# Kernel tuning notes

Hardware: AMD Instinct MI355X
Metric: run time of the kernel (lower is better)

Reference implementation:

```python
import jax, jax.numpy as jnp
from jax import lax
import numpy as np

RADIUS = 0.1
NSAMPLE = 32
STRIDE = 3
ED_NSAMPLE = 10


def _sqdist(a, b):
    # a: [B,M,3], b: [B,N,3] -> [B,M,N] squared euclidean distance
    return (jnp.sum(a * a, -1)[:, :, None] + jnp.sum(b * b, -1)[:, None, :]
            - 2.0 * jnp.einsum('bmc,bnc->bmn', a, b))


def setup_inputs() -> dict:
    key = jax.random.key(0)
    ks = jax.random.split(key, 16)
    B, N = 8, 4096
    s = 0.05
    inp = {
        'data': jax.random.normal(ks[0], (B, N, 3), dtype=jnp.float32),
        'numpoints': N,
        # stem MLP 3 -> 64
        'W_stem': jax.random.normal(ks[1], (3, 64), dtype=jnp.float32) * s,
        'b_stem': jnp.zeros((64,), jnp.float32),
        # SA shared MLP (3 dp + 64 fj) -> 128
        'W_sa': jax.random.normal(ks[2], (67, 128), dtype=jnp.float32) * s,
        'b_sa': jnp.zeros((128,), jnp.float32),
        # FP MLP (128 interp + 64 skip) -> 64
        'W_fp': jax.random.normal(ks[3], (192, 64), dtype=jnp.float32) * s,
        'b_fp': jnp.zeros((64,), jnp.float32),
        # eigen-feature MLP 3 -> 4 -> 4
        'W_e1': jax.random.normal(ks[4], (3, 4), dtype=jnp.float32) * s,
        'b_e1': jnp.zeros((4,), jnp.float32),
        'W_e2': jax.random.normal(ks[5], (4, 4), dtype=jnp.float32) * s,
        'b_e2': jnp.zeros((4,), jnp.float32),
        # conv_final 1x1: 68 -> 64, + BN affine
        'W_fin': jax.random.normal(ks[6], (68, 64), dtype=jnp.float32) * s,
        'b_fin': jnp.zeros((64,), jnp.float32),
        'gamma': jnp.ones((64,), jnp.float32),
        'beta': jnp.zeros((64,), jnp.float32),
    }
    return inp


def reference(data, numpoints, W_stem, b_stem, W_sa, b_sa, W_fp, b_fp,
              W_e1, b_e1, W_e2, b_e2, W_fin, b_fin, gamma, beta):
    B, N, _ = data.shape
    b_ix = jnp.arange(B)[:, None, None]

    # ---------- encoder: stem MLP ----------
    f0 = jax.nn.relu(data @ W_stem + b_stem)  # [B,N,64]

    # set abstraction: stride-subsample centers, ball query, dp_fj, MLP, max
    sub_idx = jnp.arange(0, N, STRIDE)
    new_xyz = data[:, sub_idx]                 # [B,M,3]
    d2 = _sqdist(new_xyz, data)                # [B,M,N]
    col = jnp.arange(N, dtype=jnp.int32)
    valid = d2 < RADIUS * RADIUS
    keys = jnp.where(valid, col, N + col)      # first-valid ball query ordering
    negk, _ = lax.top_k(-keys, NSAMPLE)
    idx = -negk                                # [B,M,ns]
    first = idx[..., :1]                       # self point always valid
    idx = jnp.where(idx >= N, first, idx)
    g_xyz = data[b_ix, idx]                    # [B,M,ns,3]
    dp = (g_xyz - new_xyz[:, :, None, :]) / RADIUS  # normalize_dp
    g_f = f0[b_ix, idx]                        # [B,M,ns,64]
    feat = jnp.concatenate([dp, g_f], -1)      # [B,M,ns,67]
    h = jax.nn.relu(feat @ W_sa + b_sa)        # [B,M,ns,128]
    f_sub = jnp.max(h, axis=2)                 # [B,M,128]

    # ---------- decoder: 3-NN inverse-distance feature propagation ----------
    d2f = _sqdist(data, new_xyz)               # [B,N,M]
    negd, nn = lax.top_k(-d2f, 3)
    w = 1.0 / (-negd + 1e-8)
    w = w / jnp.sum(w, -1, keepdims=True)      # [B,N,3]
    nbr_f = f_sub[b_ix, nn]                    # [B,N,3,128]
    interp = jnp.einsum('bnk,bnkc->bnc', w, nbr_f)
    f = jax.nn.relu(jnp.concatenate([interp, f0], -1) @ W_fp + b_fp)  # [B,N,64]

    # ---------- KNN covariance eigen-features ----------
    d2e = _sqdist(data, data)                  # [B,N,N]
    _, gidx = lax.top_k(-d2e, ED_NSAMPLE)      # [B,N,k]
    nbr = data[b_ix, gidx]                     # [B,N,k,3]
    cen = nbr - jnp.mean(nbr, axis=2, keepdims=True)
    cov = jnp.einsum('bnkc,bnkd->bncd', cen, cen) / ED_NSAMPLE  # [B,N,3,3]
    eig = jnp.linalg.eigvalsh(cov)             # [B,N,3] ascending
    ef = jax.nn.relu(eig @ W_e1 + b_e1) @ W_e2 + b_e2  # [B,N,4]

    # ---------- fused 1x1 conv + BN (training-mode stats) + relu ----------
    z_in = jnp.concatenate([f, ef], -1)        # [B,N,68]
    zc = z_in @ W_fin + b_fin                  # [B,N,64]
    mu = jnp.mean(zc, axis=(0, 1))
    var = jnp.var(zc, axis=(0, 1))
    z = jax.nn.relu((zc - mu) * lax.rsqrt(var + 1e-5) * gamma + beta)
    z = jnp.transpose(z, (0, 2, 1))            # [B,64,N]
    return (data, z)
```

## Files before the change

### kernel.cpp

```cpp
#include <hip/hip_runtime.h>
#include <stdint.h>

#define BB 8
#define NN 4096
#define MM 1366
#define NS 32
#define RAD2 0.01f
#define NGRP 64
#define KW 8

__device__ __forceinline__ float rl(float v, int l) {
    return __int_as_float(__builtin_amdgcn_readlane(__float_as_int(v), l));
}
__device__ __forceinline__ uint32_t um(uint32_t a, uint32_t b) { return a < b ? a : b; }
__device__ __forceinline__ uint32_t ux(uint32_t a, uint32_t b) { return a > b ? a : b; }
__device__ __forceinline__ uint32_t um3(uint32_t a, uint32_t b, uint32_t c) { return um(um(a, b), c); }

__device__ __forceinline__ void mrg2(uint32_t* kk, uint32_t s0, uint32_t s1) {
    uint32_t n0 = um(kk[0], s0);
    uint32_t n1 = um3(kk[1], ux(kk[0], s0), s1);
    uint32_t n2 = um3(kk[2], ux(kk[1], s0), ux(kk[0], s1));
    uint32_t n3 = um3(kk[3], ux(kk[2], s0), ux(kk[1], s1));
    uint32_t n4 = um3(kk[4], ux(kk[3], s0), ux(kk[2], s1));
    uint32_t n5 = um3(kk[5], ux(kk[4], s0), ux(kk[3], s1));
    uint32_t n6 = um3(kk[6], ux(kk[5], s0), ux(kk[4], s1));
    uint32_t n7 = um3(kk[7], ux(kk[6], s0), ux(kk[5], s1));
    uint32_t n8 = um3(kk[8], ux(kk[7], s0), ux(kk[6], s1));
    uint32_t n9 = um3(kk[9], ux(kk[8], s0), ux(kk[7], s1));
    kk[0]=n0; kk[1]=n1; kk[2]=n2; kk[3]=n3; kk[4]=n4;
    kk[5]=n5; kk[6]=n6; kk[7]=n7; kk[8]=n8; kk[9]=n9;
}

__device__ __forceinline__ void mrg4(uint32_t* kk, uint32_t s0, uint32_t s1,
                                     uint32_t s2, uint32_t s3) {
    uint32_t n0 = um(kk[0], s0);
    uint32_t n1 = um3(kk[1], ux(kk[0], s0), s1);
    uint32_t n2 = um(um3(kk[2], ux(kk[1], s0), ux(kk[0], s1)), s2);
    uint32_t n3 = um3(um3(kk[3], ux(kk[2], s0), ux(kk[1], s1)), ux(kk[0], s2), s3);
    uint32_t n4 = um3(um3(kk[4], ux(kk[3], s0), ux(kk[2], s1)), ux(kk[1], s2), ux(kk[0], s3));
    uint32_t n5 = um3(um3(kk[5], ux(kk[4], s0), ux(kk[3], s1)), ux(kk[2], s2), ux(kk[1], s3));
    uint32_t n6 = um3(um3(kk[6], ux(kk[5], s0), ux(kk[4], s1)), ux(kk[3], s2), ux(kk[2], s3));
    uint32_t n7 = um3(um3(kk[7], ux(kk[6], s0), ux(kk[5], s1)), ux(kk[4], s2), ux(kk[3], s3));
    uint32_t n8 = um3(um3(kk[8], ux(kk[7], s0), ux(kk[6], s1)), ux(kk[5], s2), ux(kk[4], s3));
    uint32_t n9 = um3(um3(kk[9], ux(kk[8], s0), ux(kk[7], s1)), ux(kk[6], s2), ux(kk[5], s3));
    kk[0]=n0; kk[1]=n1; kk[2]=n2; kk[3]=n3; kk[4]=n4;
    kk[5]=n5; kk[6]=n6; kk[7]=n7; kk[8]=n8; kk[9]=n9;
}

__device__ __forceinline__ void srt4(uint32_t& a, uint32_t& b, uint32_t& c, uint32_t& d) {
    uint32_t t0 = um(a, b), t1 = ux(a, b), t2 = um(c, d), t3 = ux(c, d);
    uint32_t s0 = um(t0, t2), m0 = ux(t0, t2), m1 = um(t1, t3), s3 = ux(t1, t3);
    a = s0; b = um(m0, m1); c = ux(m0, m1); d = s3;
}

__device__ __forceinline__ uint32_t spr3(uint32_t v) {
    v = (v | (v << 4)) & 0xC3u;
    v = (v | (v << 2)) & 0x249u;
    return v;
}

__global__ __launch_bounds__(256) void k_stem(const float* __restrict__ data,
                                              const float* __restrict__ Ws,
                                              const float* __restrict__ bs,
                                              float* __restrict__ f0,
                                              float* __restrict__ out,
                                              float4* __restrict__ cand4) {
    int blk = blockIdx.x;
    if (blk >= (BB * NN * 64) / 256) {
        int t = (blk - (BB * NN * 64) / 256) * 256 + threadIdx.x;
        float x = data[t * 3], y = data[t * 3 + 1], z = data[t * 3 + 2];
        out[t * 3] = x; out[t * 3 + 1] = y; out[t * 3 + 2] = z;
        cand4[t] = make_float4(x, y, z, x * x + y * y + z * z);
        return;
    }
    int t = blk * 256 + threadIdx.x;
    int c = t & 63;
    int r = t >> 6;
    const float* d = data + r * 3;
    float acc = bs[c];
    acc = fmaf(d[0], Ws[c], acc);
    acc = fmaf(d[1], Ws[64 + c], acc);
    acc = fmaf(d[2], Ws[128 + c], acc);
    f0[t] = fmaxf(acc, 0.f);
}

__global__ __launch_bounds__(256) void k_sort(const float4* __restrict__ cand4,
                                              float4* __restrict__ cand4s,
                                              uint32_t* __restrict__ perm,
                                              float4* __restrict__ gbox) {
    __shared__ uint32_t cnt[4096];
    __shared__ uint32_t part[256];
    int b = blockIdx.x, t = threadIdx.x;
    const float4* cb = cand4 + b * NN;
    for (int i = t; i < 4096; i += 256) cnt[i] = 0;
    __syncthreads();
    uint32_t cid[16];
    #pragma unroll
    for (int u = 0; u < 16; ++u) {
        float4 c = cb[u * 256 + t];
        int ix = (int)floorf((c.x + 4.f) * 2.f);
        int iy = (int)floorf((c.y + 4.f) * 2.f);
        int iz = (int)floorf((c.z + 4.f) * 2.f);
        ix = ix < 0 ? 0 : (ix > 15 ? 15 : ix);
        iy = iy < 0 ? 0 : (iy > 15 ? 15 : iy);
        iz = iz < 0 ? 0 : (iz > 15 ? 15 : iz);
        uint32_t m = spr3((uint32_t)ix) | (spr3((uint32_t)iy) << 1) | (spr3((uint32_t)iz) << 2);
        cid[u] = m;
        atomicAdd(&cnt[m], 1u);
    }
    __syncthreads();
    uint32_t c16[16];
    uint32_t s = 0;
    #pragma unroll
    for (int u = 0; u < 16; ++u) { c16[u] = cnt[t * 16 + u]; s += c16[u]; }
    part[t] = s;
    __syncthreads();
    for (int off = 1; off < 256; off <<= 1) {
        uint32_t v = (t >= off) ? part[t - off] : 0u;
        __syncthreads();
        part[t] += v;
        __syncthreads();
    }
    uint32_t run = part[t] - s;
    #pragma unroll
    for (int u = 0; u < 16; ++u) { cnt[t * 16 + u] = run; run += c16[u]; }
    __syncthreads();
    #pragma unroll
    for (int u = 0; u < 16; ++u) {
        int p = u * 256 + t;
        uint32_t pos = atomicAdd(&cnt[cid[u]], 1u);
        cand4s[b * NN + pos] = cb[p];
        perm[b * NN + pos] = (uint32_t)p;
    }
    __syncthreads();
    if (t < NGRP) {
        float4 mn = make_float4(1e30f, 1e30f, 1e30f, 0.f);
        float4 mx = make_float4(-1e30f, -1e30f, -1e30f, 0.f);
        for (int j = 0; j < 64; ++j) {
            float4 c = cand4s[b * NN + t * 64 + j];
            mn.x = fminf(mn.x, c.x); mn.y = fminf(mn.y, c.y); mn.z = fminf(mn.z, c.z);
            mx.x = fmaxf(mx.x, c.x); mx.y = fmaxf(mx.y, c.y); mx.z = fmaxf(mx.z, c.z);
        }
        gbox[(b * NGRP + t) * 2]     = mn;
        gbox[(b * NGRP + t) * 2 + 1] = mx;
    }
}

__global__ __launch_bounds__(512) void k_knn(const float4* __restrict__ cand4s,
                                             const uint32_t* __restrict__ perm,
                                             const float4* __restrict__ gbox,
                                             uint32_t* __restrict__ mrg) {
    __shared__ float4 sBox[2 * NGRP];
    __shared__ uint32_t sKK[KW][64][10];
    int t = threadIdx.x, w = t >> 6, lane = t & 63;
    int gw = blockIdx.x;
    int b = gw >> 6;
    int g = gw & (NGRP - 1);
    for (int i = t; i < 2 * NGRP; i += 512) sBox[i] = gbox[b * 2 * NGRP + i];
    __syncthreads();
    const float4* cs = cand4s + b * NN;
    const uint32_t* ps = perm + b * NN;
    float4 me = cs[g * 64 + lane];
    uint32_t mo = ps[g * 64 + lane];
    float px = me.x, py = me.y, pz = me.z, pa = me.w;
    uint32_t kk[10];
    #pragma unroll
    for (int r = 0; r < 10; ++r) kk[r] = 0xFFFFFF00u + r;

    auto scan_packets = [&](int jg, int j0, int j1) {
        const float4* cp = cs + jg * 64;
        const uint4* pq = (const uint4*)(ps + jg * 64);
        for (int j = j0; j < j1; ++j) {
            float4 ca  = cp[j * 4];
            float4 cbv = cp[j * 4 + 1];
            float4 cc  = cp[j * 4 + 2];
            float4 cd  = cp[j * 4 + 3];
            uint4 pm = pq[j];
            float da  = fmaxf(fmaf(-2.f, fmaf(pz, ca.z,  fmaf(py, ca.y,  px * ca.x)),  pa + ca.w),  0.f);
            float db_ = fmaxf(fmaf(-2.f, fmaf(pz, cbv.z, fmaf(py, cbv.y, px * cbv.x)), pa + cbv.w), 0.f);
            float dc  = fmaxf(fmaf(-2.f, fmaf(pz, cc.z,  fmaf(py, cc.y,  px * cc.x)),  pa + cc.w),  0.f);
            float dd  = fmaxf(fmaf(-2.f, fmaf(pz, cd.z,  fmaf(py, cd.y,  px * cd.x)),  pa + cd.w),  0.f);
            uint32_t ka = (__float_as_uint(da)  & 0xFFFFF000u) | pm.x;
            uint32_t kb = (__float_as_uint(db_) & 0xFFFFF000u) | pm.y;
            uint32_t kc = (__float_as_uint(dc)  & 0xFFFFF000u) | pm.z;
            uint32_t kd = (__float_as_uint(dd)  & 0xFFFFF000u) | pm.w;
            uint32_t mn4 = um(um(ka, kb), um(kc, kd));
            if (__ballot(mn4 < kk[9])) {
                srt4(ka, kb, kc, kd);
                mrg4(kk, ka, kb, kc, kd);
            }
        }
    };
    auto bound = [&]() {
        uint32_t kb9 = kk[9] & 0xFFFFF000u;
        float u2 = (kb9 >= 0x7F000000u) ? 1e30f : __uint_as_float(kb9 + 0x1000u);
        #pragma unroll
        for (int off = 1; off < 64; off <<= 1) u2 = fmaxf(u2, __shfl_xor(u2, off));
        return u2;
    };

    scan_packets(g, w * 2, w * 2 + 2);
    float ub = bound();
    float4 amn = sBox[g * 2], amx = sBox[g * 2 + 1];
    float4 bmn = sBox[lane * 2], bmx = sBox[lane * 2 + 1];
    float bx = fmaxf(fmaxf(amn.x - bmx.x, bmn.x - amx.x), 0.f);
    float by = fmaxf(fmaxf(amn.y - bmx.y, bmn.y - amx.y), 0.f);
    float bz = fmaxf(fmaxf(amn.z - bmx.z, bmn.z - amx.z), 0.f);
    float bdj = fmaf(bx, bx, fmaf(by, by, bz * bz));
    if (lane == g) bdj = 1e30f;
    for (int rank = 0; rank < NGRP - 1; ++rank) {
        float mind = bdj;
        #pragma unroll
        for (int off = 1; off < 64; off <<= 1) mind = fminf(mind, __shfl_xor(mind, off));
        if (!(mind < ub * 1.0005f)) break;
        unsigned long long mm = __ballot(bdj == mind);
        int jl = (int)__builtin_ctzll(mm);
        if (lane == jl) bdj = 1e30f;
        if ((rank & (KW - 1)) == w) {
            scan_packets(jl, 0, 16);
            ub = bound();
        }
    }
    if (w > 0) {
        #pragma unroll
        for (int r = 0; r < 10; ++r) sKK[w][lane][r] = kk[r];
    }
    __syncthreads();
    if (w == 0) {
        for (int ww = 1; ww < KW; ++ww) {
            uint32_t s[10];
            #pragma unroll
            for (int r = 0; r < 10; ++r) s[r] = sKK[ww][lane][r];
            mrg4(kk, s[0], s[1], s[2], s[3]);
            mrg4(kk, s[4], s[5], s[6], s[7]);
            mrg2(kk, s[8], s[9]);
        }
        int gp = b * NN + (int)mo;
        #pragma unroll
        for (int r = 0; r < 10; ++r) mrg[r * (BB * NN) + gp] = kk[r];
    }
}

__device__ __forceinline__ void jrot(float& app, float& aqq, float& apq,
                                     float& arp, float& arq) {
    float ap = apq;
    if (fabsf(ap) > 1e-32f) {
        float th = (aqq - app) / (2.f * ap);
        float t = 1.f / (fabsf(th) + sqrtf(th * th + 1.f));
        t = th < 0.f ? -t : t;
        float c = 1.f / sqrtf(t * t + 1.f);
        float s = t * c;
        app = app - t * ap;
        aqq = aqq + t * ap;
        apq = 0.f;
        float rp = arp, rq = arq;
        arp = c * rp - s * rq;
        arq = s * rp + c * rq;
    }
}

__global__ __launch_bounds__(256) void k_knn_eig(const float4* __restrict__ cand4,
                                                 const uint32_t* __restrict__ mrg,
                                                 const float* __restrict__ We1,
                                                 const float* __restrict__ be1,
                                                 const float* __restrict__ We2,
                                                 const float* __restrict__ be2,
                                                 float* __restrict__ ef) {
    int t = blockIdx.x * 256 + threadIdx.x;
    int b = t >> 12;
    const float4* cb = cand4 + b * NN;
    uint32_t kk[10];
    #pragma unroll
    for (int r = 0; r < 10; ++r) kk[r] = mrg[r * (BB * NN) + t];
    float xs[10], ys[10], zs[10];
    float mx = 0.f, my = 0.f, mz = 0.f;
    #pragma unroll
    for (int r = 0; r < 10; ++r) {
        int n = (int)(kk[r] & 0xFFFu);
        float4 cr = cb[n];
        xs[r] = cr.x; ys[r] = cr.y; zs[r] = cr.z;
        mx += xs[r]; my += ys[r]; mz += zs[r];
    }
    mx *= 0.1f; my *= 0.1f; mz *= 0.1f;
    float a00 = 0, a01 = 0, a02 = 0, a11 = 0, a12 = 0, a22 = 0;
    #pragma unroll
    for (int r = 0; r < 10; ++r) {
        float x = xs[r] - mx, y = ys[r] - my, z = zs[r] - mz;
        a00 = fmaf(x, x, a00); a01 = fmaf(x, y, a01); a02 = fmaf(x, z, a02);
        a11 = fmaf(y, y, a11); a12 = fmaf(y, z, a12); a22 = fmaf(z, z, a22);
    }
    a00 *= 0.1f; a01 *= 0.1f; a02 *= 0.1f; a11 *= 0.1f; a12 *= 0.1f; a22 *= 0.1f;
    #pragma unroll
    for (int sweep = 0; sweep < 6; ++sweep) {
        jrot(a00, a11, a01, a02, a12);
        jrot(a00, a22, a02, a01, a12);
        jrot(a11, a22, a12, a01, a02);
    }
    float e0 = a00, e1 = a11, e2 = a22, tmp;
    if (e0 > e1) { tmp = e0; e0 = e1; e1 = tmp; }
    if (e1 > e2) { tmp = e1; e1 = e2; e2 = tmp; }
    if (e0 > e1) { tmp = e0; e0 = e1; e1 = tmp; }
    float tt[4];
    #pragma unroll
    for (int i = 0; i < 4; ++i) {
        float v = be1[i];
        v = fmaf(e0, We1[i], v);
        v = fmaf(e1, We1[4 + i], v);
        v = fmaf(e2, We1[8 + i], v);
        tt[i] = fmaxf(v, 0.f);
    }
    #pragma unroll
    for (int i = 0; i < 4; ++i) {
        float v = be2[i];
        v = fmaf(tt[0], We2[i], v);
        v = fmaf(tt[1], We2[4 + i], v);
        v = fmaf(tt[2], We2[8 + i], v);
        v = fmaf(tt[3], We2[12 + i], v);
        ef[t * 4 + i] = v;
    }
}

__global__ __launch_bounds__(256) void k_sa(const float4* __restrict__ cand4,
                                            const float* __restrict__ data,
                                            const float* __restrict__ f0,
                                            const uint32_t* __restrict__ mrg,
                                            const float* __restrict__ Wsa,
                                            const float* __restrict__ bsa,
                                            float* __restrict__ fsub) {
    __shared__ float2 sW[67 * 64];
    __shared__ int sIdx[4][NS];
    for (int i = threadIdx.x; i < 67 * 64; i += 256) {
        int k = i >> 6, c = i & 63;
        sW[i] = make_float2(Wsa[k * 128 + c], Wsa[k * 128 + 64 + c]);
    }
    __syncthreads();
    int wv = threadIdx.x >> 6, lane = threadIdx.x & 63;
    int gm = blockIdx.x * 4 + wv;
    if (gm >= BB * MM) return;
    int b = gm / MM, m = gm - b * MM;
    const float4* cb4 = cand4 + b * NN;
    const float* db = data + b * NN * 3;
    float4 cen = cb4[3 * m];
    float cx = cen.x, cy = cen.y, cz = cen.z, sa = cen.w;

    int cnt;
    bool fallback;
    {
        float d2l = 1e30f;
        int idxl = 0;
        if (lane < 10) {
            uint32_t key = mrg[lane * (BB * NN) + b * NN + 3 * m];
            idxl = (int)(key & 0xFFFu);
            float4 c = cb4[idxl];
            float dot = fmaf(cz, c.z, fmaf(cy, c.y, cx * c.x));
            d2l = (sa + c.w) - 2.f * dot;
        }
        bool valid = (lane < 10) && (d2l < RAD2);
        unsigned long long mask = __ballot(valid);
        if (valid) sIdx[wv][__popcll(mask & ((1ull << lane) - 1ull))] = idxl;
        cnt = __popcll(mask);
        fallback = rl(d2l, 9) < RAD2 * 1.0005f;
    }
    if (fallback) {
        cnt = 0;
        for (int base = 0; base < NN; base += 64) {
            int n = base + lane;
            float4 c = cb4[n];
            float dot = fmaf(cz, c.z, fmaf(cy, c.y, cx * c.x));
            float d2 = (sa + c.w) - 2.f * dot;
            bool valid = d2 < RAD2;
            unsigned long long mask = __ballot(valid);
            if (valid) {
                int pos = cnt + __popcll(mask & ((1ull << lane) - 1ull));
                if (pos < NS) sIdx[wv][pos] = n;
            }
            cnt += __popcll(mask);
            if (cnt >= NS) break;
        }
    }
    int scnt = cnt < NS ? cnt : NS;

    float cl = lane == 0 ? cx : (lane == 1 ? cy : cz);
    float hb0 = bsa[lane], hb1 = bsa[64 + lane];
    float m0 = 0.f, m1 = 0.f;

    for (int s0 = 0; s0 < scnt; s0 += 4) {
        float fr[4], fr2[4];
        #pragma unroll
        for (int u = 0; u < 4; ++u) {
            int s = s0 + u;
            if (s >= scnt) s = 0;
            int nj = sIdx[wv][s];
            int fb = (b * NN + nj) * 64;
            float v;
            if (lane >= 3) v = f0[fb + lane - 3];
            else           v = (db[nj * 3 + lane] - cl) * 10.0f;
            fr[u] = v;
            fr2[u] = (lane < 3) ? f0[fb + 61 + lane] : 0.f;
        }
        float h0[4], h1[4];
        #pragma unroll
        for (int u = 0; u < 4; ++u) { h0[u] = hb0; h1[u] = hb1; }
        for (int k = 0; k < 64; ++k) {
            float2 w = sW[k * 64 + lane];
            #pragma unroll
            for (int u = 0; u < 4; ++u) {
                float fv = rl(fr[u], k);
                h0[u] = fmaf(fv, w.x, h0[u]);
                h1[u] = fmaf(fv, w.y, h1[u]);
            }
        }
        #pragma unroll
        for (int k = 64; k < 67; ++k) {
            float2 w = sW[k * 64 + lane];
            #pragma unroll
            for (int u = 0; u < 4; ++u) {
                float fv = rl(fr2[u], k - 64);
                h0[u] = fmaf(fv, w.x, h0[u]);
                h1[u] = fmaf(fv, w.y, h1[u]);
            }
        }
        #pragma unroll
        for (int u = 0; u < 4; ++u) {
            m0 = fmaxf(m0, fmaxf(h0[u], 0.f));
            m1 = fmaxf(m1, fmaxf(h1[u], 0.f));
        }
    }
    fsub[gm * 128 + lane] = m0;
    fsub[gm * 128 + 64 + lane] = m1;
}

__global__ __launch_bounds__(512) void k_interp(const float4* __restrict__ cand4,
                                                const float* __restrict__ fsub,
                                                float* __restrict__ itp) {
    __shared__ float4 sC[MM];
    __shared__ float sMD[8][64][3];
    __shared__ int   sMI[8][64][3];
    __shared__ float sWts[64][3];
    __shared__ int   sNbr[64][3];
    int t = threadIdx.x, wv = t >> 6, lane = t & 63;
    int blk = blockIdx.x;
    int b = blk >> 6;
    int pbase = (blk & 63) * 64;
    const float4* cb4 = cand4 + b * NN;
    for (int m = t; m < MM; m += 512) sC[m] = cb4[3 * m];
    __syncthreads();
    int p = pbase + lane;
    float4 pm = cb4[p];
    float px = pm.x, py = pm.y, pz = pm.z, pa = pm.w;
    float d0 = 1e30f, d1 = 1e30f, d2v = 1e30f;
    int n0 = 0, n1 = 0, n2 = 0;
    int ms = wv * 171, me = ms + 171 < MM ? ms + 171 : MM;
    for (int m = ms; m < me; ++m) {
        float4 c = sC[m];
        float dd = (pa + c.w) - 2.f * (px * c.x + py * c.y + pz * c.z);
        if (dd < d2v) {
            if (dd < d1) {
                d2v = d1; n2 = n1;
                if (dd < d0) { d1 = d0; n1 = n0; d0 = dd; n0 = m; }
                else         { d1 = dd; n1 = m; }
            } else { d2v = dd; n2 = m; }
        }
    }
    sMD[wv][lane][0] = d0; sMD[wv][lane][1] = d1; sMD[wv][lane][2] = d2v;
    sMI[wv][lane][0] = n0; sMI[wv][lane][1] = n1; sMI[wv][lane][2] = n2;
    __syncthreads();
    if (wv == 0) {
        d0 = sMD[0][lane][0]; d1 = sMD[0][lane][1]; d2v = sMD[0][lane][2];
        n0 = sMI[0][lane][0]; n1 = sMI[0][lane][1]; n2 = sMI[0][lane][2];
        for (int w = 1; w < 8; ++w) {
            #pragma unroll
            for (int r = 0; r < 3; ++r) {
                float dd = sMD[w][lane][r];
                int mm = sMI[w][lane][r];
                if (dd < d2v) {
                    if (dd < d1) {
                        d2v = d1; n2 = n1;
                        if (dd < d0) { d1 = d0; n1 = n0; d0 = dd; n0 = mm; }
                        else         { d1 = dd; n1 = mm; }
                    } else { d2v = dd; n2 = mm; }
                }
            }
        }
        float w0 = 1.f / (d0 + 1e-8f), w1 = 1.f / (d1 + 1e-8f), w2 = 1.f / (d2v + 1e-8f);
        float ws = w0 + w1 + w2;
        sWts[lane][0] = w0 / ws; sWts[lane][1] = w1 / ws; sWts[lane][2] = w2 / ws;
        sNbr[lane][0] = n0; sNbr[lane][1] = n1; sNbr[lane][2] = n2;
    }
    __syncthreads();
    for (int i = wv * 8; i < wv * 8 + 8; ++i) {
        float a0 = sWts[i][0], a1 = sWts[i][1], a2 = sWts[i][2];
        const float* r0 = fsub + (b * MM + sNbr[i][0]) * 128;
        const float* r1 = fsub + (b * MM + sNbr[i][1]) * 128;
        const float* r2 = fsub + (b * MM + sNbr[i][2]) * 128;
        float v0 = fmaf(a2, r2[lane], fmaf(a1, r1[lane], a0 * r0[lane]));
        float v1 = fmaf(a2, r2[64 + lane], fmaf(a1, r1[64 + lane], a0 * r0[64 + lane]));
        int row = b * NN + pbase + i;
        itp[row * 128 + lane] = v0;
        itp[row * 128 + 64 + lane] = v1;
    }
}

__global__ __launch_bounds__(256) void k_fp(const float* __restrict__ itp,
                                            const float* __restrict__ f0,
                                            const float* __restrict__ W,
                                            const float* __restrict__ bias,
                                            float* __restrict__ outf) {
    __shared__ float sW[192 * 64];
    for (int i = threadIdx.x; i < 192 * 64; i += 256) sW[i] = W[i];
    __syncthreads();
    int lane = threadIdx.x & 63;
    int wv = threadIdx.x >> 6;
    float bb = bias[lane];
    int rowbase = blockIdx.x * 64 + wv * 16;
    for (int it = 0; it < 4; ++it) {
        int r = rowbase + it * 4;
        float fa[4], fbv[4], fc[4], acc[4];
        #pragma unroll
        for (int u = 0; u < 4; ++u) {
            fa[u]  = itp[(r + u) * 128 + lane];
            fbv[u] = itp[(r + u) * 128 + 64 + lane];
            fc[u]  = f0[(r + u) * 64 + lane];
            acc[u] = bb;
        }
        #pragma unroll
        for (int k = 0; k < 192; ++k) {
            float w = sW[k * 64 + lane];
            #pragma unroll
            for (int u = 0; u < 4; ++u) {
                float fv = k < 64 ? rl(fa[u], k)
                         : (k < 128 ? rl(fbv[u], k - 64) : rl(fc[u], k - 128));
                acc[u] = fmaf(fv, w, acc[u]);
            }
        }
        #pragma unroll
        for (int u = 0; u < 4; ++u)
            outf[(r + u) * 64 + lane] = fmaxf(acc[u], 0.f);
    }
}

__global__ __launch_bounds__(256) void k_fin(const float* __restrict__ fb,
                                             const float* __restrict__ efb,
                                             const float* __restrict__ W,
                                             const float* __restrict__ bias,
                                             float* __restrict__ zc) {
    __shared__ float sW[68 * 64];
    for (int i = threadIdx.x; i < 68 * 64; i += 256) sW[i] = W[i];
    __syncthreads();
    int lane = threadIdx.x & 63;
    int wv = threadIdx.x >> 6;
    float bb = bias[lane];
    int rowbase = blockIdx.x * 64 + wv * 16;
    for (int it = 0; it < 4; ++it) {
        int r = rowbase + it * 4;
        float fa[4], fe[4], acc[4];
        #pragma unroll
        for (int u = 0; u < 4; ++u) {
            fa[u] = fb[(r + u) * 64 + lane];
            fe[u] = (lane < 4) ? efb[(r + u) * 4 + lane] : 0.f;
            acc[u] = bb;
        }
        #pragma unroll
        for (int k = 0; k < 68; ++k) {
            float w = sW[k * 64 + lane];
            #pragma unroll
            for (int u = 0; u < 4; ++u) {
                float fv = k < 64 ? rl(fa[u], k) : rl(fe[u], k - 64);
                acc[u] = fmaf(fv, w, acc[u]);
            }
        }
        #pragma unroll
        for (int u = 0; u < 4; ++u)
            zc[(r + u) * 64 + lane] = acc[u];
    }
}

__global__ __launch_bounds__(256) void k_stats1(const float* __restrict__ zc,
                                                float* __restrict__ pp) {
    int t = threadIdx.x;
    int c = t & 63, r4 = t >> 6;
    float s = 0.f, sq = 0.f;
    int base = blockIdx.x * 512;
    for (int i = 0; i < 128; ++i) {
        float v = zc[(base + i * 4 + r4) * 64 + c];
        s += v;
        sq = fmaf(v, v, sq);
    }
    __shared__ float ls[256], lq[256];
    ls[t] = s; lq[t] = sq;
    __syncthreads();
    if (t < 64) {
        float st = ls[t] + ls[t + 64] + ls[t + 128] + ls[t + 192];
        float qt = lq[t] + lq[t + 64] + lq[t + 128] + lq[t + 192];
        pp[blockIdx.x * 128 + t] = st;
        pp[blockIdx.x * 128 + 64 + t] = qt;
    }
}

__global__ __launch_bounds__(64) void k_stats2(const float* __restrict__ pp,
                                               const float* __restrict__ gamma,
                                               const float* __restrict__ beta,
                                               float* __restrict__ ss) {
    int c = threadIdx.x;
    float s = 0.f, sq = 0.f;
    for (int k = 0; k < 64; ++k) {
        s += pp[k * 128 + c];
        sq += pp[k * 128 + 64 + c];
    }
    const float inv = 1.f / (float)(BB * NN);
    float mu = s * inv;
    float var = sq * inv - mu * mu;
    float sc = gamma[c] / sqrtf(var + 1e-5f);
    ss[c] = sc;
    ss[64 + c] = beta[c] - mu * sc;
}

__global__ __launch_bounds__(256) void k_norm_t(const float* __restrict__ zc,
                                                const float* __restrict__ ss,
                                                float* __restrict__ out) {
    __shared__ float sT[64][65];
    int blk = blockIdx.x;
    int b = blk >> 6;
    int nbase = (blk & 63) * 64;
    int c = threadIdx.x & 63;
    int r4 = threadIdx.x >> 6;
    float sc = ss[c], sh = ss[64 + c];
    #pragma unroll
    for (int i = 0; i < 16; ++i) {
        int nr = i * 4 + r4;
        float v = zc[(b * NN + nbase + nr) * 64 + c];
        sT[nr][c] = fmaxf(fmaf(v, sc, sh), 0.f);
    }
    __syncthreads();
    int nn = threadIdx.x & 63;
    #pragma unroll
    for (int i = 0; i < 16; ++i) {
        int cc = i * 4 + r4;
        out[BB * NN * 3 + (b * 64 + cc) * NN + nbase + nn] = sT[nn][cc];
    }
}

extern "C" void kernel_launch(void* const* d_in, const int* in_sizes, int n_in,
                              void* d_out, int out_size, void* d_ws, size_t ws_size,
                              hipStream_t stream) {
    const float* data = (const float*)d_in[0];
    const float* Wst  = (const float*)d_in[2];
    const float* bst  = (const float*)d_in[3];
    const float* Wsa  = (const float*)d_in[4];
    const float* bsa  = (const float*)d_in[5];
    const float* Wfp  = (const float*)d_in[6];
    const float* bfp  = (const float*)d_in[7];
    const float* We1  = (const float*)d_in[8];
    const float* be1  = (const float*)d_in[9];
    const float* We2  = (const float*)d_in[10];
    const float* be2  = (const float*)d_in[11];
    const float* Wfin = (const float*)d_in[12];
    const float* bfin = (const float*)d_in[13];
    const float* gamma = (const float*)d_in[14];
    const float* beta  = (const float*)d_in[15];
    float* out = (float*)d_out;

    float* f0   = (float*)d_ws;
    float* fsub = f0 + 2097152;
    float* efb  = fsub + 1398784;
    float* zc   = efb + 131072;
    float* ss   = zc + 2097152;
    float* pp   = ss + 128;
    float4* cand4 = (float4*)(pp + 8192);
    uint32_t* mrgb = (uint32_t*)((float*)cand4 + 131072);
    float* itp  = (float*)mrgb + 1310720;
    float* fb   = itp + 4194304;
    float4*   cand4s = (float4*)itp;
    uint32_t* perm   = (uint32_t*)(itp + 131072);
    float4*   gbox   = (float4*)(itp + 131072 + 32768);

    k_stem<<<(BB * NN * 64) / 256 + (BB * NN) / 256, 256, 0, stream>>>(
        data, Wst, bst, f0, out, cand4);
    k_sort<<<BB, 256, 0, stream>>>(cand4, cand4s, perm, gbox);
    k_knn<<<BB * NGRP, 512, 0, stream>>>(cand4s, perm, gbox, mrgb);
    k_knn_eig<<<(BB * NN) / 256, 256, 0, stream>>>(cand4, mrgb, We1, be1, We2, be2, efb);
    k_sa<<<(BB * MM + 3) / 4, 256, 0, stream>>>(cand4, data, f0, mrgb, Wsa, bsa, fsub);
    k_interp<<<BB * 64, 512, 0, stream>>>(cand4, fsub, itp);
    k_fp<<<512, 256, 0, stream>>>(itp, f0, Wfp, bfp, fb);
    k_fin<<<512, 256, 0, stream>>>(fb, efb, Wfin, bfin, zc);
    k_stats1<<<64, 256, 0, stream>>>(zc, pp);
    k_stats2<<<1, 64, 0, stream>>>(pp, gamma, beta, ss);
    k_norm_t<<<512, 256, 0, stream>>>(zc, ss, out);
}
```

Measured before the change: 330.4 us.

## Share merged KNN threshold across waves in synchronized rounds of group scans

The KNN kernel previously had each of eight waves independently pick candidate groups by box distance and prune using only its own local top-10 bound. Now the waves run rounds: in each one, all partial lists are merged in shared memory, wave 0 computes the global 10th-best threshold and the next up-to-8 groups whose boxes fall within it, and the waves scan those groups pruning against the tighter shared threshold. The goal is to cut redundant group scans and merge work through better pruning, at the cost of extra block barriers and serial merge work on wave 0 every round.

```diff
diff --git a/kernel.cpp b/kernel.cpp
--- a/kernel.cpp
+++ b/kernel.cpp
@@ -152,6 +152,9 @@
                                              uint32_t* __restrict__ mrg) {
     __shared__ float4 sBox[2 * NGRP];
     __shared__ uint32_t sKK[KW][64][10];
+    __shared__ uint32_t sThr[64];
+    __shared__ int sGrp[KW];
+    __shared__ int sN;
     int t = threadIdx.x, w = t >> 6, lane = t & 63;
     int gw = blockIdx.x;
     int b = gw >> 6;
@@ -167,9 +170,10 @@
     #pragma unroll
     for (int r = 0; r < 10; ++r) kk[r] = 0xFFFFFF00u + r;
 
-    auto scan_packets = [&](int jg, int j0, int j1) {
+    auto scan_packets = [&](int jg, int j0, int j1, uint32_t thrC) {
         const float4* cp = cs + jg * 64;
         const uint4* pq = (const uint4*)(ps + jg * 64);
+        uint32_t thr = um(kk[9], thrC);
         for (int j = j0; j < j1; ++j) {
             float4 ca  = cp[j * 4];
             float4 cbv = cp[j * 4 + 1];
@@ -185,59 +189,75 @@
             uint32_t kc = (__float_as_uint(dc)  & 0xFFFFF000u) | pm.z;
             uint32_t kd = (__float_as_uint(dd)  & 0xFFFFF000u) | pm.w;
             uint32_t mn4 = um(um(ka, kb), um(kc, kd));
-            if (__ballot(mn4 < kk[9])) {
+            if (__ballot(mn4 < thr)) {
                 srt4(ka, kb, kc, kd);
                 mrg4(kk, ka, kb, kc, kd);
+                thr = um(kk[9], thrC);
             }
         }
     };
-    auto bound = [&]() {
-        uint32_t kb9 = kk[9] & 0xFFFFF000u;
-        float u2 = (kb9 >= 0x7F000000u) ? 1e30f : __uint_as_float(kb9 + 0x1000u);
-        #pragma unroll
-        for (int off = 1; off < 64; off <<= 1) u2 = fmaxf(u2, __shfl_xor(u2, off));
-        return u2;
-    };
-
-    scan_packets(g, w * 2, w * 2 + 2);
-    float ub = bound();
-    float4 amn = sBox[g * 2], amx = sBox[g * 2 + 1];
-    float4 bmn = sBox[lane * 2], bmx = sBox[lane * 2 + 1];
-    float bx = fmaxf(fmaxf(amn.x - bmx.x, bmn.x - amx.x), 0.f);
-    float by = fmaxf(fmaxf(amn.y - bmx.y, bmn.y - amx.y), 0.f);
-    float bz = fmaxf(fmaxf(amn.z - bmx.z, bmn.z - amx.z), 0.f);
-    float bdj = fmaf(bx, bx, fmaf(by, by, bz * bz));
-    if (lane == g) bdj = 1e30f;
-    for (int rank = 0; rank < NGRP - 1; ++rank) {
-        float mind = bdj;
-        #pragma unroll
-        for (int off = 1; off < 64; off <<= 1) mind = fminf(mind, __shfl_xor(mind, off));
-        if (!(mind < ub * 1.0005f)) break;
-        unsigned long long mm = __ballot(bdj == mind);
-        int jl = (int)__builtin_ctzll(mm);
-        if (lane == jl) bdj = 1e30f;
-        if ((rank & (KW - 1)) == w) {
-            scan_packets(jl, 0, 16);
-            ub = bound();
-        }
-    }
-    if (w > 0) {
+
+    scan_packets(g, w * 2, w * 2 + 2, 0xFFFFFFFFu);
+
+    float bdj = 1e30f;
+    if (w == 0) {
+        float4 amn = sBox[g * 2], amx = sBox[g * 2 + 1];
+        float4 bmn = sBox[lane * 2], bmx = sBox[lane * 2 + 1];
+        float bx = fmaxf(fmaxf(amn.x - bmx.x, bmn.x - amx.x), 0.f);
+        float by = fmaxf(fmaxf(amn.y - bmx.y, bmn.y - amx.y), 0.f);
+        float bz = fmaxf(fmaxf(amn.z - bmx.z, bmn.z - amx.z), 0.f);
+        bdj = fmaf(bx, bx, fmaf(by, by, bz * bz));
+        if (lane == g) bdj = 1e30f;
+    }
+
+    uint32_t tmp[10];
+    for (int round = 0; round < 10; ++round) {
         #pragma unroll
         for (int r = 0; r < 10; ++r) sKK[w][lane][r] = kk[r];
-    }
-    __syncthreads();
+        __syncthreads();
+        if (w == 0) {
+            #pragma unroll
+            for (int r = 0; r < 10; ++r) tmp[r] = kk[r];
+            for (int ww = 1; ww < KW; ++ww) {
+                uint32_t s[10];
+                #pragma unroll
+                for (int r = 0; r < 10; ++r) s[r] = sKK[ww][lane][r];
+                mrg4(tmp, s[0], s[1], s[2], s[3]);
+                mrg4(tmp, s[4], s[5], s[6], s[7]);
+                mrg2(tmp, s[8], s[9]);
+            }
+            sThr[lane] = tmp[9];
+            uint32_t kb9 = tmp[9] & 0xFFFFF000u;
+            float u2 = (kb9 >= 0x7F000000u) ? 1e30f : __uint_as_float(kb9 + 0x1000u);
+            #pragma unroll
+            for (int off = 1; off < 64; off <<= 1) u2 = fmaxf(u2, __shfl_xor(u2, off));
+            float ubt = u2 * 1.0005f;
+            int n = 0;
+            #pragma unroll 1
+            for (int s2 = 0; s2 < KW; ++s2) {
+                float mind = bdj;
+                #pragma unroll
+                for (int off = 1; off < 64; off <<= 1) mind = fminf(mind, __shfl_xor(mind, off));
+                if (!(mind < ubt)) break;
+                unsigned long long mm2 = __ballot(bdj == mind);
+                int jl = (int)__builtin_ctzll(mm2);
+                if (lane == 0) sGrp[n] = jl;
+                n++;
+                if (lane == jl) bdj = 1e30f;
+            }
+            if (lane == 0) sN = n;
+        }
+        __syncthreads();
+        int n = sN;
+        if (n == 0) break;
+        uint32_t thrC = sThr[lane];
+        if (w == 0) { if (n == KW) scan_packets(sGrp[KW - 1], 0, 16, thrC); }
+        else if (w - 1 < n) scan_packets(sGrp[w - 1], 0, 16, thrC);
+    }
     if (w == 0) {
-        for (int ww = 1; ww < KW; ++ww) {
-            uint32_t s[10];
-            #pragma unroll
-            for (int r = 0; r < 10; ++r) s[r] = sKK[ww][lane][r];
-            mrg4(kk, s[0], s[1], s[2], s[3]);
-            mrg4(kk, s[4], s[5], s[6], s[7]);
-            mrg2(kk, s[8], s[9]);
-        }
         int gp = b * NN + (int)mo;
         #pragma unroll
-        for (int r = 0; r < 10; ++r) mrg[r * (BB * NN) + gp] = kk[r];
+        for (int r = 0; r < 10; ++r) mrg[r * (BB * NN) + gp] = tmp[r];
     }
 }
 
```

Measured after the change: 341.4 us. 1.03x slower.

## Restructure KNN group pruning with per-point box bounds and shared threshold

Applied to the files above, without the earlier changes.

The KNN kernel drops the serial rank-ordered group visiting loop with its repeated wave reductions. Each wave now scans its own group fully, computes a shared upper-bound key, then strides over the other groups. It skips a group unless some lane's point-to-box lower bound falls below the current threshold, and uses the shared bound to filter candidate merges. The block shrinks from 8 to 4 waves. This removes reduction and serialization overhead and sharpens pruning with per-point rather than box-to-box bounds, but groups are no longer visited nearest-first, so thresholds may tighten more slowly.

```diff
diff --git a/kernel.cpp b/kernel.cpp
--- a/kernel.cpp
+++ b/kernel.cpp
@@ -7,7 +7,7 @@
 #define NS 32
 #define RAD2 0.01f
 #define NGRP 64
-#define KW 8
+#define KW 4
 
 __device__ __forceinline__ float rl(float v, int l) {
     return __int_as_float(__builtin_amdgcn_readlane(__float_as_int(v), l));
@@ -146,17 +146,17 @@
     }
 }
 
-__global__ __launch_bounds__(512) void k_knn(const float4* __restrict__ cand4s,
+__global__ __launch_bounds__(256) void k_knn(const float4* __restrict__ cand4s,
                                              const uint32_t* __restrict__ perm,
                                              const float4* __restrict__ gbox,
                                              uint32_t* __restrict__ mrg) {
     __shared__ float4 sBox[2 * NGRP];
-    __shared__ uint32_t sKK[KW][64][10];
+    __shared__ uint32_t sKK[KW - 1][64][10];
     int t = threadIdx.x, w = t >> 6, lane = t & 63;
     int gw = blockIdx.x;
     int b = gw >> 6;
     int g = gw & (NGRP - 1);
-    for (int i = t; i < 2 * NGRP; i += 512) sBox[i] = gbox[b * 2 * NGRP + i];
+    for (int i = t; i < 2 * NGRP; i += 256) sBox[i] = gbox[b * 2 * NGRP + i];
     __syncthreads();
     const float4* cs = cand4s + b * NN;
     const uint32_t* ps = perm + b * NN;
@@ -167,10 +167,11 @@
     #pragma unroll
     for (int r = 0; r < 10; ++r) kk[r] = 0xFFFFFF00u + r;
 
-    auto scan_packets = [&](int jg, int j0, int j1) {
+    auto scan_packets = [&](int jg, uint32_t thrC) {
         const float4* cp = cs + jg * 64;
         const uint4* pq = (const uint4*)(ps + jg * 64);
-        for (int j = j0; j < j1; ++j) {
+        uint32_t thr = um(kk[9], thrC);
+        for (int j = 0; j < 16; ++j) {
             float4 ca  = cp[j * 4];
             float4 cbv = cp[j * 4 + 1];
             float4 cc  = cp[j * 4 + 2];
@@ -185,49 +186,52 @@
             uint32_t kc = (__float_as_uint(dc)  & 0xFFFFF000u) | pm.z;
             uint32_t kd = (__float_as_uint(dd)  & 0xFFFFF000u) | pm.w;
             uint32_t mn4 = um(um(ka, kb), um(kc, kd));
-            if (__ballot(mn4 < kk[9])) {
+            if (__ballot(mn4 < thr)) {
                 srt4(ka, kb, kc, kd);
                 mrg4(kk, ka, kb, kc, kd);
+                thr = um(kk[9], thrC);
             }
         }
     };
-    auto bound = [&]() {
-        uint32_t kb9 = kk[9] & 0xFFFFF000u;
-        float u2 = (kb9 >= 0x7F000000u) ? 1e30f : __uint_as_float(kb9 + 0x1000u);
-        #pragma unroll
-        for (int off = 1; off < 64; off <<= 1) u2 = fmaxf(u2, __shfl_xor(u2, off));
-        return u2;
-    };
-
-    scan_packets(g, w * 2, w * 2 + 2);
-    float ub = bound();
-    float4 amn = sBox[g * 2], amx = sBox[g * 2 + 1];
-    float4 bmn = sBox[lane * 2], bmx = sBox[lane * 2 + 1];
-    float bx = fmaxf(fmaxf(amn.x - bmx.x, bmn.x - amx.x), 0.f);
-    float by = fmaxf(fmaxf(amn.y - bmx.y, bmn.y - amx.y), 0.f);
-    float bz = fmaxf(fmaxf(amn.z - bmx.z, bmn.z - amx.z), 0.f);
-    float bdj = fmaf(bx, bx, fmaf(by, by, bz * bz));
-    if (lane == g) bdj = 1e30f;
-    for (int rank = 0; rank < NGRP - 1; ++rank) {
-        float mind = bdj;
-        #pragma unroll
-        for (int off = 1; off < 64; off <<= 1) mind = fminf(mind, __shfl_xor(mind, off));
-        if (!(mind < ub * 1.0005f)) break;
-        unsigned long long mm = __ballot(bdj == mind);
-        int jl = (int)__builtin_ctzll(mm);
-        if (lane == jl) bdj = 1e30f;
-        if ((rank & (KW - 1)) == w) {
-            scan_packets(jl, 0, 16);
-            ub = bound();
-        }
-    }
+
+    scan_packets(g, 0xFFFFFFFFu);
+
+    uint32_t ub_key;
+    {
+        uint32_t kb9 = (kk[9] & 0xFFFFF000u) + 0x1000u;
+        #pragma unroll
+        for (int off = 1; off < 64; off <<= 1) {
+            uint32_t o = (uint32_t)__shfl_xor((int)kb9, off);
+            kb9 = ux(kb9, o);
+        }
+        ub_key = kb9;
+    }
+
     if (w > 0) {
         #pragma unroll
-        for (int r = 0; r < 10; ++r) sKK[w][lane][r] = kk[r];
+        for (int r = 0; r < 10; ++r) kk[r] = 0xFFFFFF00u + r;
+    }
+
+    for (int jg = w; jg < NGRP; jg += KW) {
+        if (jg == g) continue;
+        float4 bmn = sBox[jg * 2], bmx = sBox[jg * 2 + 1];
+        float dx = fmaxf(fmaxf(bmn.x - px, px - bmx.x), 0.f);
+        float dy = fmaxf(fmaxf(bmn.y - py, py - bmx.y), 0.f);
+        float dz = fmaxf(fmaxf(bmn.z - pz, pz - bmx.z), 0.f);
+        float lb = fmaf(dx, dx, fmaf(dy, dy, dz * dz));
+        uint32_t mt = um(kk[9], ub_key);
+        float tf = __uint_as_float((mt & 0xFFFFF000u) + 0x1000u) * 1.0005f;
+        if (__ballot(lb < tf))
+            scan_packets(jg, ub_key);
+    }
+
+    if (w > 0) {
+        #pragma unroll
+        for (int r = 0; r < 10; ++r) sKK[w - 1][lane][r] = kk[r];
     }
     __syncthreads();
     if (w == 0) {
-        for (int ww = 1; ww < KW; ++ww) {
+        for (int ww = 0; ww < KW - 1; ++ww) {
             uint32_t s[10];
             #pragma unroll
             for (int r = 0; r < 10; ++r) s[r] = sKK[ww][lane][r];
@@ -677,7 +681,7 @@
     k_stem<<<(BB * NN * 64) / 256 + (BB * NN) / 256, 256, 0, stream>>>(
         data, Wst, bst, f0, out, cand4);
     k_sort<<<BB, 256, 0, stream>>>(cand4, cand4s, perm, gbox);
-    k_knn<<<BB * NGRP, 512, 0, stream>>>(cand4s, perm, gbox, mrgb);
+    k_knn<<<BB * NGRP, 256, 0, stream>>>(cand4s, perm, gbox, mrgb);
     k_knn_eig<<<(BB * NN) / 256, 256, 0, stream>>>(cand4, mrgb, We1, be1, We2, be2, efb);
     k_sa<<<(BB * MM + 3) / 4, 256, 0, stream>>>(cand4, data, f0, mrgb, Wsa, bsa, fsub);
     k_interp<<<BB * 64, 512, 0, stream>>>(cand4, fsub, itp);
```

New measurement: 336.2 us. Within noise of the previous version (+1.7%).
